# Optimization experiments

Hardware: AMD Instinct MI355X
Metric: run time of the kernel (lower is better)

Reference implementation:

```python
import jax, jax.numpy as jnp
import numpy as np

B, T, S = 4, 4096, 4096
D_MODEL = 512        # d_query = d_value_in = d_key_in
N_HEADS = 8
D_KEY = 512
D_VALUE = 512
N_OMEGA = 64
EPS = 1e-9
DK_H = D_KEY // N_HEADS      # 64
DV_H = D_VALUE // N_HEADS    # 64


def _glorot(key, shape):
    fan_in, fan_out = shape[-2], shape[-1]
    lim = np.sqrt(6.0 / (fan_in + fan_out))
    return jax.random.uniform(key, shape, jnp.float32, -lim, lim)


def _draw_omega(key, d_feature, n_omega):
    # n_omega == d_feature here -> single orthogonal block scaled by sqrt(d)
    g = jax.random.normal(key, (d_feature, d_feature), jnp.float32)
    q, _ = jnp.linalg.qr(g)
    q = q * jnp.sqrt(jnp.float32(d_feature))
    return q[:n_omega]


def setup_inputs() -> dict:
    key = jax.random.key(0)
    ks = jax.random.split(key, 7)
    return {
        "query": 0.5 * jax.random.normal(ks[0], (B, T, D_MODEL), jnp.float32),
        "value": 0.5 * jax.random.normal(ks[1], (B, S, D_MODEL), jnp.float32),
        "key": 0.5 * jax.random.normal(ks[2], (B, S, D_MODEL), jnp.float32),
        "wq": _glorot(ks[3], (N_HEADS, D_MODEL, DK_H)),
        "wv": _glorot(ks[4], (N_HEADS, D_MODEL, DV_H)),
        "wk": _glorot(ks[5], (N_HEADS, D_MODEL, DK_H)),
        "omega": _draw_omega(ks[6], DK_H, N_OMEGA),
    }


def _phi(x, omega):
    # x: (B,H,T,dk_h) -> (B,H,T,2*n_omega) FAVOR+ positive random features
    square_sum = 0.5 * jnp.sum(x * x, axis=-1, keepdims=True)
    xw = jnp.einsum('bhtk,mk->bhtm', x, omega)
    un = jnp.exp(jnp.concatenate([xw, -xw], axis=-1) - square_sum) + EPS
    return un / jnp.sqrt(jnp.float32(2.0 * N_OMEGA))


def reference(query, value, key, wq, wv, wk, omega):
    q = jnp.einsum('btf,hfk->bhtk', query, wq)   # (B,H,T,dk_h)
    v = jnp.einsum('bsd,hdk->bhsk', value, wv)   # (B,H,S,dv_h)
    k = jnp.einsum('bsf,hfk->bhsk', key, wk)     # (B,H,S,dk_h)
    qp = _phi(q, omega)                          # (B,H,T,2M)
    kp = _phi(k, omega)                          # (B,H,S,2M)
    v1 = jnp.concatenate([v, jnp.ones(v.shape[:-1] + (1,), v.dtype)], axis=-1)
    kv = jnp.einsum('bhsm,bhsd->bhmd', kp, v1)   # (B,H,2M,dv_h+1)
    qkv = jnp.einsum('bhtm,bhmd->bhtd', qp, kv)  # (B,H,T,dv_h+1)
    normalizer = qkv[..., -1:]
    out = qkv[..., :-1] / normalizer
    # faithful to original: plain reshape (B,H,T,dv_h) -> (B,T,D_VALUE), no transpose
    return jnp.reshape(out, (B, T, D_VALUE))
```

## Files before the change

kernel.cpp:

```cpp
#include <hip/hip_runtime.h>

typedef _Float16 half8 __attribute__((ext_vector_type(8)));
typedef _Float16 half4_t __attribute__((ext_vector_type(4)));
typedef short short8 __attribute__((ext_vector_type(8)));
typedef unsigned short u16x4 __attribute__((ext_vector_type(4)));
typedef float f32x4 __attribute__((ext_vector_type(4)));

#define NH 8

__device__ __forceinline__ unsigned short f2bf(float x) {
  union { float f; unsigned u; } v; v.f = x;
  unsigned r = v.u + 0x7FFFu + ((v.u >> 16) & 1u);
  return (unsigned short)(r >> 16);
}

#define DRAIN_BAR()                                  \
  asm volatile("s_waitcnt lgkmcnt(0)" ::: "memory"); \
  __builtin_amdgcn_s_barrier();                      \
  __builtin_amdgcn_sched_barrier(0)

__global__ __launch_bounds__(256) void k0_qk(
    const float* __restrict__ wq, const float* __restrict__ wk,
    const float* __restrict__ omega,
    _Float16* __restrict__ wxq, _Float16* __restrict__ wxk) {
  const int bid = blockIdx.x;
  const int arr = bid >> 7;
  const int h = (bid >> 4) & 7;
  const int ft = (bid >> 1) & 7;
  const int os = bid & 1;
  const int f = threadIdx.x & 63;
  const int w = threadIdx.x >> 6;
  const float* wsrc = (arr ? wk : wq) + ((size_t)h * 512 + ft * 64 + f) * 64;
  float wreg[64];
#pragma unroll
  for (int i = 0; i < 16; ++i) {
    float4 v = *(const float4*)(wsrc + i * 4);
    wreg[i * 4] = v.x; wreg[i * 4 + 1] = v.y; wreg[i * 4 + 2] = v.z; wreg[i * 4 + 3] = v.w;
  }
  _Float16* outp = arr ? wxk : wxq;
  const int k8 = f >> 3, e = f & 7;
#pragma unroll 1
  for (int oo = 0; oo < 8; ++oo) {
    const int o = w * 16 + os * 8 + oo;
    const float* om = omega + o * 64;
    float s = 0.f;
#pragma unroll
    for (int k = 0; k < 64; ++k) s = fmaf(wreg[k], om[k], s);
    outp[((((size_t)h * 8 + ft) * 8 + k8) * 64 + o) * 8 + e] = (_Float16)s;
  }
}

__global__ __launch_bounds__(256) void k0_v(
    const float* __restrict__ wv, _Float16* __restrict__ wvt) {
  int idx = blockIdx.x * 256 + threadIdx.x;
  int h = idx >> 15, o = (idx >> 9) & 63, f = idx & 511;
  float val = wv[((size_t)h * 512 + f) * 64 + o];
  wvt[((((size_t)h * 8 + (f >> 6)) * 8 + ((f >> 3) & 7)) * 64 + o) * 8 + (f & 7)] = (_Float16)val;
}

__global__ __launch_bounds__(512, 1) void fused_kv(
    const float* __restrict__ key, const float* __restrict__ value,
    const _Float16* __restrict__ wxk, const _Float16* __restrict__ wvt,
    float* __restrict__ kvpart) {
  __shared__ __align__(16) _Float16 A[2][128][72];
  __shared__ __align__(16) _Float16 W[2][2][4096];
  __shared__ __align__(16) unsigned short kpT[128][136];
  __shared__ __align__(16) unsigned short vT[64][136];
  const int bid = blockIdx.x;
  const int hp = bid >> 6;
  const int b = (bid >> 4) & 3;
  const int sc = bid & 15;
  const int s0 = sc * 256;
  const int tid = threadIdx.x;
  const int w = tid >> 6;
  const int lane = tid & 63;
  const int g = lane >> 4, c = lane & 15;
  const int hh = w >> 2;
  const int rq = w & 3;
  const int xr = lane >> 4;
  const int xc = (lane & 15) * 4;

  const _Float16* wkb0 = wxk + (size_t)(hp * 2) * 32768;
  const _Float16* wkb1 = wkb0 + 32768;
  const _Float16* wvb0 = wvt + (size_t)(hp * 2) * 32768;
  const _Float16* wvb1 = wvb0 + 32768;

  short8 bones;
#pragma unroll
  for (int i = 0; i < 8; ++i) bones[i] = (c == 0) ? (short)0x3F80 : (short)0;

  f32x4 acc_kv[2][5];
#pragma unroll
  for (int h2 = 0; h2 < 2; ++h2)
#pragma unroll
    for (int j = 0; j < 5; ++j) acc_kv[h2][j] = (f32x4){0.f, 0.f, 0.f, 0.f};

  u16x4 kps[2][4], kms[2][4], vs_[2][4];

  float4 xv[4];
  half8 wr0, wr1;

#pragma unroll 1
  for (int p = 0; p < 4; ++p) {
    const float* xb = ((p & 1) ? value : key) +
                      (size_t)(b * 4096 + s0 + (p >> 1) * 128 + w * 16 + xr) * 512 + xc;
    const _Float16* wb0 = (p & 1) ? wvb0 : wkb0;
    const _Float16* wb1 = (p & 1) ? wvb1 : wkb1;

#pragma unroll
    for (int i = 0; i < 4; ++i) xv[i] = *(const float4*)(xb + i * 2048);
    wr0 = *(const half8*)(wb0 + tid * 8);
    wr1 = *(const half8*)(wb1 + tid * 8);
#pragma unroll
    for (int i = 0; i < 4; ++i) {
      float vv[4] = {xv[i].x, xv[i].y, xv[i].z, xv[i].w};
      half4_t hv;
#pragma unroll
      for (int j2 = 0; j2 < 4; ++j2) hv[j2] = (_Float16)vv[j2];
      *(half4_t*)&A[0][w * 16 + i * 4 + xr][xc] = hv;
    }
    *(half8*)&W[0][0][tid * 8] = wr0;
    *(half8*)&W[0][1][tid * 8] = wr1;
#pragma unroll
    for (int i = 0; i < 4; ++i) xv[i] = *(const float4*)(xb + 64 + i * 2048);
    wr0 = *(const half8*)(wb0 + 4096 + tid * 8);
    wr1 = *(const half8*)(wb1 + 4096 + tid * 8);
    DRAIN_BAR();

    f32x4 accp[2][4];
#pragma unroll
    for (int mf = 0; mf < 2; ++mf)
#pragma unroll
      for (int j = 0; j < 4; ++j) accp[mf][j] = (f32x4){0.f, 0.f, 0.f, 0.f};

#pragma unroll 1
    for (int kc = 0; kc < 8; ++kc) {
      const int cur = kc & 1;
      if (kc < 7) {
        const int nxt = cur ^ 1;
#pragma unroll
        for (int i = 0; i < 4; ++i) {
          float vv[4] = {xv[i].x, xv[i].y, xv[i].z, xv[i].w};
          half4_t hv;
#pragma unroll
          for (int j2 = 0; j2 < 4; ++j2) hv[j2] = (_Float16)vv[j2];
          *(half4_t*)&A[nxt][w * 16 + i * 4 + xr][xc] = hv;
        }
        *(half8*)&W[nxt][0][tid * 8] = wr0;
        *(half8*)&W[nxt][1][tid * 8] = wr1;
        if (kc < 6) {
#pragma unroll
          for (int i = 0; i < 4; ++i)
            xv[i] = *(const float4*)(xb + (kc + 2) * 64 + i * 2048);
          wr0 = *(const half8*)(wb0 + (kc + 2) * 4096 + tid * 8);
          wr1 = *(const half8*)(wb1 + (kc + 2) * 4096 + tid * 8);
        }
      }
#pragma unroll
      for (int ks = 0; ks < 2; ++ks) {
        half8 af0 = *(const half8*)&A[cur][rq * 32 + c][ks * 32 + g * 8];
        half8 af1 = *(const half8*)&A[cur][rq * 32 + 16 + c][ks * 32 + g * 8];
#pragma unroll
        for (int nf = 0; nf < 4; ++nf) {
          half8 wf = *(const half8*)&W[cur][hh][((ks * 4 + g) * 64 + nf * 16 + c) * 8];
          accp[0][nf] = __builtin_amdgcn_mfma_f32_16x16x32_f16(af0, wf, accp[0][nf], 0, 0, 0);
          accp[1][nf] = __builtin_amdgcn_mfma_f32_16x16x32_f16(af1, wf, accp[1][nf], 0, 0, 0);
        }
      }
      DRAIN_BAR();
    }

    if ((p & 1) == 0) {
#pragma unroll
      for (int mf = 0; mf < 2; ++mf) {
        float ss_[4];
#pragma unroll
        for (int j = 0; j < 4; ++j) {
          float s = 0.f;
#pragma unroll
          for (int nf = 0; nf < 4; ++nf) { float q = accp[mf][nf][j]; s = fmaf(q, q, s); }
          s += __shfl_xor(s, 1); s += __shfl_xor(s, 2);
          s += __shfl_xor(s, 4); s += __shfl_xor(s, 8);
          ss_[j] = s * 0.0078125f;
        }
#pragma unroll
        for (int nf = 0; nf < 4; ++nf) {
          u16x4 kp_p, kp_m;
#pragma unroll
          for (int j = 0; j < 4; ++j) {
            float v = accp[mf][nf][j];
            kp_p[j] = f2bf(__expf(v - ss_[j]) + 1e-9f);
            kp_m[j] = f2bf(__expf(-v - ss_[j]) + 1e-9f);
          }
          kps[mf][nf] = kp_p;
          kms[mf][nf] = kp_m;
        }
      }
    } else {
#pragma unroll
      for (int mf = 0; mf < 2; ++mf)
#pragma unroll
        for (int nf = 0; nf < 4; ++nf) {
          u16x4 vv;
#pragma unroll
          for (int j = 0; j < 4; ++j) vv[j] = f2bf(accp[mf][nf][j]);
          vs_[mf][nf] = vv;
        }
#pragma unroll
      for (int h2 = 0; h2 < 2; ++h2) {
        if (hh == h2) {
#pragma unroll
          for (int mf = 0; mf < 2; ++mf)
#pragma unroll
            for (int nf = 0; nf < 4; ++nf) {
              const int m = nf * 16 + c;
              const int sl = rq * 32 + mf * 16 + g * 4;
              *(u16x4*)&kpT[m][sl] = kps[mf][nf];
              *(u16x4*)&kpT[64 + m][sl] = kms[mf][nf];
              *(u16x4*)&vT[m][sl] = vs_[mf][nf];
            }
        }
        DRAIN_BAR();
#pragma unroll
        for (int ks = 0; ks < 4; ++ks) {
          short8 a = *(const short8*)&kpT[w * 16 + c][ks * 32 + g * 8];
#pragma unroll
          for (int nf = 0; nf < 4; ++nf) {
            short8 bb = *(const short8*)&vT[nf * 16 + c][ks * 32 + g * 8];
            acc_kv[h2][nf] = __builtin_amdgcn_mfma_f32_16x16x32_bf16(a, bb, acc_kv[h2][nf], 0, 0, 0);
          }
          acc_kv[h2][4] = __builtin_amdgcn_mfma_f32_16x16x32_bf16(a, bones, acc_kv[h2][4], 0, 0, 0);
        }
        __builtin_amdgcn_s_barrier();
      }
    }
  }

#pragma unroll
  for (int h2 = 0; h2 < 2; ++h2) {
    float* pbase = kvpart + ((size_t)sc * 32 + b * 8 + hp * 2 + h2) * 10240;
#pragma unroll
    for (int nf = 0; nf < 5; ++nf)
#pragma unroll
      for (int j = 0; j < 4; ++j)
        pbase[(w * 16 + g * 4 + j) * 80 + nf * 16 + c] = acc_kv[h2][nf][j];
  }
}

__global__ __launch_bounds__(128) void k3a_denom(
    const float* __restrict__ kvpart, float* __restrict__ invbuf,
    float* __restrict__ lsc) {
  const int bh = blockIdx.x;
  const int m = threadIdx.x;
  const float* base = kvpart + (size_t)bh * 10240 + m * 80 + 64;
  float s = 0.f;
#pragma unroll
  for (int kk = 0; kk < 16; ++kk) s += base[(size_t)kk * 327680];
  invbuf[bh * 128 + m] = 1.0f / s;
  lsc[bh * 128 + m] = __logf(s);
}

__global__ __launch_bounds__(256) void k3b_reduce(
    const float* __restrict__ kvpart, const float* __restrict__ invbuf,
    _Float16* __restrict__ kvnt) {
  const int bh = blockIdx.x;
  const int e0 = blockIdx.y * 1024 + threadIdx.x * 4;
  const int m = e0 / 80;
  const int d0 = e0 - m * 80;
  const float* base = kvpart + (size_t)bh * 10240 + e0;
  f32x4 s = (f32x4){0.f, 0.f, 0.f, 0.f};
#pragma unroll
  for (int kk = 0; kk < 16; ++kk) {
    f32x4 v = *(const f32x4*)(base + (size_t)kk * 327680);
    s += v;
  }
  const float inv = invbuf[bh * 128 + m];
  const int mst = ((m & 63) << 1) | (m >> 6);
  _Float16* outb = kvnt + (size_t)bh * 10240 + mst;
#pragma unroll
  for (int j = 0; j < 4; ++j) {
    const int d = d0 + j;
    float val;
    if (d < 64) val = s[j] * inv;
    else if (d == 64) val = 1.0f;
    else val = 0.f;
    outb[d * 128] = (_Float16)val;
  }
}

__global__ __launch_bounds__(256, 2) void fused_qo(
    const float* __restrict__ query, const _Float16* __restrict__ wxq,
    const _Float16* __restrict__ kvnt, const float* __restrict__ lsc,
    float* __restrict__ out) {
  __shared__ __align__(16) _Float16 A_[64][136];
  const int bid = blockIdx.x;
  const int hh2 = bid >> 8;
  const int b = (bid >> 6) & 3;
  const int tt = bid & 63;
  const int t0 = tt * 64;
  const int tid = threadIdx.x;
  const int w = tid >> 6;
  const int lane = tid & 63;
  const int g = lane >> 4, c = lane & 15;
  const int arow = tid >> 2;
  const int acb = (tid & 3) * 32;

  const float* xq = query + (size_t)(b * 4096 + t0 + arow) * 512 + acb;

  f32x4 accp[4][4];
#pragma unroll
  for (int h = 0; h < 4; ++h)
#pragma unroll
    for (int j = 0; j < 4; ++j) accp[h][j] = (f32x4){0.f, 0.f, 0.f, 0.f};

  float4 xv[8];
  half8 wregs[3][8];

#define ISSUE_WREG(S)                                                         \
  do {                                                                        \
    const int kq_ = (S) >> 3, loc_ = (S) & 7, h_ = loc_ >> 1, kc2_ = loc_ & 1;\
    const _Float16* ws =                                                      \
        wxq + ((size_t)(hh2 * 4 + h_) * 8 + kq_ * 2 + kc2_) * 4096;           \
    _Pragma("unroll")                                                         \
    for (int r = 0; r < 8; ++r) {                                             \
      const int ks_ = r >> 2, nf_ = r & 3;                                    \
      wregs[(S) % 3][r] =                                                     \
          *(const half8*)(ws + (((ks_ * 4 + g) * 64) + nf_ * 16 + c) * 8);    \
    }                                                                         \
  } while (0)

#pragma unroll
  for (int i = 0; i < 8; ++i) xv[i] = *(const float4*)(xq + i * 4);
  ISSUE_WREG(0);
  ISSUE_WREG(1);

#pragma unroll
  for (int kq = 0; kq < 4; ++kq) {
    if (kq > 0) { DRAIN_BAR(); }
#pragma unroll
    for (int i = 0; i < 8; i += 2) {
      half8 hv;
      hv[0] = (_Float16)xv[i].x;     hv[1] = (_Float16)xv[i].y;
      hv[2] = (_Float16)xv[i].z;     hv[3] = (_Float16)xv[i].w;
      hv[4] = (_Float16)xv[i + 1].x; hv[5] = (_Float16)xv[i + 1].y;
      hv[6] = (_Float16)xv[i + 1].z; hv[7] = (_Float16)xv[i + 1].w;
      *(half8*)&A_[arow][acb + i * 4] = hv;
    }
    if (kq < 3) {
#pragma unroll
      for (int i = 0; i < 8; ++i)
        xv[i] = *(const float4*)(xq + (kq + 1) * 128 + i * 4);
    }
    DRAIN_BAR();

#pragma unroll
    for (int loc = 0; loc < 8; ++loc) {
      const int S = kq * 8 + loc;
      if (S + 2 < 32) ISSUE_WREG(S + 2);
      const int h = loc >> 1;
      const int kc2 = loc & 1;
#pragma unroll
      for (int ks = 0; ks < 2; ++ks) {
        half8 a = *(const half8*)&A_[w * 16 + c][kc2 * 64 + ks * 32 + g * 8];
#pragma unroll
        for (int nf = 0; nf < 4; ++nf) {
          accp[h][nf] = __builtin_amdgcn_mfma_f32_16x16x32_f16(
              a, wregs[S % 3][ks * 4 + nf], accp[h][nf], 0, 0, 0);
        }
      }
    }
  }
#undef ISSUE_WREG

  DRAIN_BAR();

#pragma unroll
  for (int h = 0; h < 4; ++h) {
    const int bh = b * NH + hh2 * 4 + h;
    float Lp[4], Lm[4];
#pragma unroll
    for (int nf = 0; nf < 4; ++nf) {
      Lp[nf] = lsc[bh * 128 + nf * 16 + c];
      Lm[nf] = lsc[bh * 128 + 64 + nf * 16 + c];
    }
    float ss_[4], cm_[4];
#pragma unroll
    for (int j = 0; j < 4; ++j) {
      float s = 0.f;
#pragma unroll
      for (int nf = 0; nf < 4; ++nf) { float q = accp[h][nf][j]; s = fmaf(q, q, s); }
      s += __shfl_xor(s, 1); s += __shfl_xor(s, 2);
      s += __shfl_xor(s, 4); s += __shfl_xor(s, 8);
      ss_[j] = s * 0.0078125f;
    }
#pragma unroll
    for (int j = 0; j < 4; ++j) {
      float m0 = -1e30f;
#pragma unroll
      for (int nf = 0; nf < 4; ++nf) {
        float v = accp[h][nf][j];
        m0 = fmaxf(m0, fmaxf(v - ss_[j] + Lp[nf], -v - ss_[j] + Lm[nf]));
        m0 = fmaxf(m0, fmaxf(Lp[nf], Lm[nf]) - 20.723265f);
      }
      m0 = fmaxf(m0, __shfl_xor(m0, 1)); m0 = fmaxf(m0, __shfl_xor(m0, 2));
      m0 = fmaxf(m0, __shfl_xor(m0, 4)); m0 = fmaxf(m0, __shfl_xor(m0, 8));
      cm_[j] = m0;
    }
#pragma unroll
    for (int nf = 0; nf < 4; ++nf) {
      const int m = nf * 16 + c;
#pragma unroll
      for (int j = 0; j < 4; ++j) {
        float v = accp[h][nf][j];
        _Float16 pp = (_Float16)(__expf(v - ss_[j] + Lp[nf] - cm_[j]) +
                                 1e-9f * __expf(Lp[nf] - cm_[j]));
        _Float16 pm = (_Float16)(__expf(-v - ss_[j] + Lm[nf] - cm_[j]) +
                                 1e-9f * __expf(Lm[nf] - cm_[j]));
        union { unsigned u; _Float16 hh_[2]; } pk;
        pk.hh_[0] = pp; pk.hh_[1] = pm;
        *(unsigned*)&A_[w * 16 + g * 4 + j][2 * m] = pk.u;
      }
    }
    DRAIN_BAR();

    f32x4 acco[5];
#pragma unroll
    for (int j = 0; j < 5; ++j) acco[j] = (f32x4){0.f, 0.f, 0.f, 0.f};
    const _Float16* kvb = kvnt + (size_t)bh * 10240;
#pragma unroll
    for (int ks = 0; ks < 4; ++ks) {
      half8 a = *(const half8*)&A_[w * 16 + c][ks * 32 + g * 8];
#pragma unroll
      for (int nf = 0; nf < 5; ++nf) {
        half8 bb = *(const half8*)(kvb + (size_t)(nf * 16 + c) * 128 + ks * 32 + g * 8);
        acco[nf] = __builtin_amdgcn_mfma_f32_16x16x32_f16(a, bb, acco[nf], 0, 0, 0);
      }
    }
    const int tb = t0 + w * 16 + g * 4;
#pragma unroll
    for (int j = 0; j < 4; ++j) {
      float nrm = __shfl(acco[4][j], (lane & 48));
      float invn = 1.0f / nrm;
#pragma unroll
      for (int nf = 0; nf < 4; ++nf) {
        out[((size_t)bh * 4096 + tb + j) * 64 + nf * 16 + c] = acco[nf][j] * invn;
      }
    }
    DRAIN_BAR();
  }
}

extern "C" void kernel_launch(void* const* d_in, const int* in_sizes, int n_in,
                              void* d_out, int out_size, void* d_ws, size_t ws_size,
                              hipStream_t stream) {
  const float* query = (const float*)d_in[0];
  const float* value = (const float*)d_in[1];
  const float* key   = (const float*)d_in[2];
  const float* wq    = (const float*)d_in[3];
  const float* wv    = (const float*)d_in[4];
  const float* wk    = (const float*)d_in[5];
  const float* omega = (const float*)d_in[6];
  float* out = (float*)d_out;
  char* ws = (char*)d_ws;

  _Float16* wxq  = (_Float16*)(ws);
  _Float16* wxk  = (_Float16*)(ws + 524288);
  _Float16* wvt  = (_Float16*)(ws + 1048576);
  float* kvpart  = (float*)(ws + 1572864);
  _Float16* kvnt = (_Float16*)(ws + 22544384);
  float* lsc     = (float*)(ws + 23199744);
  float* invbuf  = (float*)(ws + 23216128);

  k0_qk<<<256, 256, 0, stream>>>(wq, wk, omega, wxq, wxk);
  k0_v<<<1024, 256, 0, stream>>>(wv, wvt);
  fused_kv<<<256, 512, 0, stream>>>(key, value, wxk, wvt, kvpart);
  k3a_denom<<<32, 128, 0, stream>>>(kvpart, invbuf, lsc);
  k3b_reduce<<<dim3(32, 10), 256, 0, stream>>>(kvpart, invbuf, kvnt);
  fused_qo<<<512, 256, 0, stream>>>(query, wxq, kvnt, lsc, out);
}
```

Measured before the change: 117.8 us.

## Split fused_qo into two-head blocks and stage weights through shared memory

Each fused_qo block now handles two heads instead of four, which doubles the grid to 1024 blocks and halves the accumulator registers. Weight fragments are now loaded cooperatively with coalesced per-thread loads and staged through a double-buffered LDS tile, replacing the per-lane register prefetch ring. Launch bounds are raised to 3 blocks per SIMD to get more occupancy. In exchange, each block reads the query tile once per head pair, so query traffic doubles, and every weight step adds an LDS round trip and a barrier.

```diff
diff --git a/kernel.cpp b/kernel.cpp
--- a/kernel.cpp
+++ b/kernel.cpp
@@ -288,16 +288,17 @@
   }
 }
 
-__global__ __launch_bounds__(256, 2) void fused_qo(
+__global__ __launch_bounds__(256, 3) void fused_qo(
     const float* __restrict__ query, const _Float16* __restrict__ wxq,
     const _Float16* __restrict__ kvnt, const float* __restrict__ lsc,
     float* __restrict__ out) {
   __shared__ __align__(16) _Float16 A_[64][136];
+  __shared__ __align__(16) _Float16 W2[2][4096];
   const int bid = blockIdx.x;
-  const int hh2 = bid >> 8;
-  const int b = (bid >> 6) & 3;
-  const int tt = bid & 63;
-  const int t0 = tt * 64;
+  const int hp = bid >> 8;
+  const int rt = bid & 255;
+  const int b = rt >> 6;
+  const int t0 = (rt & 63) * 64;
   const int tid = threadIdx.x;
   const int w = tid >> 6;
   const int lane = tid & 63;
@@ -307,32 +308,27 @@
 
   const float* xq = query + (size_t)(b * 4096 + t0 + arow) * 512 + acb;
 
-  f32x4 accp[4][4];
-#pragma unroll
-  for (int h = 0; h < 4; ++h)
+  f32x4 accp[2][4];
+#pragma unroll
+  for (int h = 0; h < 2; ++h)
 #pragma unroll
     for (int j = 0; j < 4; ++j) accp[h][j] = (f32x4){0.f, 0.f, 0.f, 0.f};
 
   float4 xv[8];
-  half8 wregs[3][8];
-
-#define ISSUE_WREG(S)                                                         \
-  do {                                                                        \
-    const int kq_ = (S) >> 3, loc_ = (S) & 7, h_ = loc_ >> 1, kc2_ = loc_ & 1;\
-    const _Float16* ws =                                                      \
-        wxq + ((size_t)(hh2 * 4 + h_) * 8 + kq_ * 2 + kc2_) * 4096;           \
-    _Pragma("unroll")                                                         \
-    for (int r = 0; r < 8; ++r) {                                             \
-      const int ks_ = r >> 2, nf_ = r & 3;                                    \
-      wregs[(S) % 3][r] =                                                     \
-          *(const half8*)(ws + (((ks_ * 4 + g) * 64) + nf_ * 16 + c) * 8);    \
-    }                                                                         \
+  half8 wrE[2], wrO[2];
+
+#define WSL(s) (wxq + ((size_t)(hp * 2 + (((s) & 3) >> 1)) * 8 + ((s) >> 2) * 2 + ((s) & 1)) * 4096)
+#define LOADW(r, s)                                  \
+  do {                                               \
+    const _Float16* ws_ = WSL(s);                    \
+    r[0] = *(const half8*)(ws_ + tid * 8);           \
+    r[1] = *(const half8*)(ws_ + 2048 + tid * 8);    \
   } while (0)
 
 #pragma unroll
   for (int i = 0; i < 8; ++i) xv[i] = *(const float4*)(xq + i * 4);
-  ISSUE_WREG(0);
-  ISSUE_WREG(1);
+  LOADW(wrE, 0);
+  LOADW(wrO, 1);
 
 #pragma unroll
   for (int kq = 0; kq < 4; ++kq) {
@@ -351,32 +347,40 @@
       for (int i = 0; i < 8; ++i)
         xv[i] = *(const float4*)(xq + (kq + 1) * 128 + i * 4);
     }
-    DRAIN_BAR();
-
-#pragma unroll
-    for (int loc = 0; loc < 8; ++loc) {
-      const int S = kq * 8 + loc;
-      if (S + 2 < 32) ISSUE_WREG(S + 2);
-      const int h = loc >> 1;
+#pragma unroll
+    for (int loc = 0; loc < 4; ++loc) {
+      const int S = kq * 4 + loc;
+      if ((loc & 1) == 0) {
+        *(half8*)&W2[0][tid * 8] = wrE[0];
+        *(half8*)&W2[0][2048 + tid * 8] = wrE[1];
+        if (S + 2 < 16) LOADW(wrE, S + 2);
+      } else {
+        *(half8*)&W2[1][tid * 8] = wrO[0];
+        *(half8*)&W2[1][2048 + tid * 8] = wrO[1];
+        if (S + 2 < 16) LOADW(wrO, S + 2);
+      }
+      DRAIN_BAR();
+      const int hh = loc >> 1;
       const int kc2 = loc & 1;
 #pragma unroll
       for (int ks = 0; ks < 2; ++ks) {
         half8 a = *(const half8*)&A_[w * 16 + c][kc2 * 64 + ks * 32 + g * 8];
 #pragma unroll
         for (int nf = 0; nf < 4; ++nf) {
-          accp[h][nf] = __builtin_amdgcn_mfma_f32_16x16x32_f16(
-              a, wregs[S % 3][ks * 4 + nf], accp[h][nf], 0, 0, 0);
-        }
-      }
-    }
-  }
-#undef ISSUE_WREG
+          half8 wf = *(const half8*)&W2[loc & 1][((ks * 4 + g) * 64 + nf * 16 + c) * 8];
+          accp[hh][nf] = __builtin_amdgcn_mfma_f32_16x16x32_f16(a, wf, accp[hh][nf], 0, 0, 0);
+        }
+      }
+    }
+  }
+#undef LOADW
+#undef WSL
 
   DRAIN_BAR();
 
 #pragma unroll
-  for (int h = 0; h < 4; ++h) {
-    const int bh = b * NH + hh2 * 4 + h;
+  for (int h = 0; h < 2; ++h) {
+    const int bh = b * NH + hp * 2 + h;
     float Lp[4], Lm[4];
 #pragma unroll
     for (int nf = 0; nf < 4; ++nf) {
@@ -476,5 +480,5 @@
   fused_kv<<<256, 512, 0, stream>>>(key, value, wxk, wvt, kvpart);
   k3a_denom<<<32, 128, 0, stream>>>(kvpart, invbuf, lsc);
   k3b_reduce<<<dim3(32, 10), 256, 0, stream>>>(kvpart, invbuf, kvnt);
-  fused_qo<<<512, 256, 0, stream>>>(query, wxq, kvnt, lsc, out);
-}
+  fused_qo<<<1024, 256, 0, stream>>>(query, wxq, kvnt, lsc, out);
+}
```

After: 114.3 us. 1.03x faster.
